# Kernel tuning notes

Hardware: AMD Instinct MI355X
Metric: run time of the kernel (lower is better)

The kernel has to match this reference:

```python
import jax, jax.numpy as jnp
import numpy as np
import math

GROUPS = 32  # min(256 // 4, 32)
EPS = 1e-5

def group_norm(x, w, b):
    B, C, H, W = x.shape
    xg = x.reshape(B, GROUPS, C // GROUPS, H, W)
    mean = jnp.mean(xg, axis=(2, 3, 4), keepdims=True)
    var = jnp.var(xg, axis=(2, 3, 4), keepdims=True)
    xn = ((xg - mean) * jax.lax.rsqrt(var + EPS)).reshape(B, C, H, W)
    return xn * w[None, :, None, None] + b[None, :, None, None]

def nin(x, W, b):
    # 1x1 projection: [B,C,H,W] x [C,D] -> [B,D,H,W]
    return jnp.einsum('bchw,cd->bdhw', x, W) + b[None, :, None, None]

def setup_inputs() -> dict:
    key = jax.random.key(0)
    ks = jax.random.split(key, 5)
    C = 256
    scale = 1.0 / math.sqrt(C)
    return {
        'x': jax.random.normal(ks[0], (4, C, 64, 64), dtype=jnp.float32),
        'gn_w': jnp.ones((C,), jnp.float32),
        'gn_b': jnp.zeros((C,), jnp.float32),
        'Wq': jax.random.normal(ks[1], (C, C), jnp.float32) * scale,
        'bq': jnp.zeros((C,), jnp.float32),
        'Wk': jax.random.normal(ks[2], (C, C), jnp.float32) * scale,
        'bk': jnp.zeros((C,), jnp.float32),
        'Wv': jax.random.normal(ks[3], (C, C), jnp.float32) * scale,
        'bv': jnp.zeros((C,), jnp.float32),
        'Wp': jax.random.normal(ks[4], (C, C), jnp.float32) * scale,
        'bp': jnp.zeros((C,), jnp.float32),
    }

def reference(x, gn_w, gn_b, Wq, bq, Wk, bk, Wv, bv, Wp, bp):
    B, C, H, W = x.shape
    h = group_norm(x, gn_w, gn_b)
    q = nin(h, Wq, bq).reshape(B, C, H * W)
    k = nin(h, Wk, bk).reshape(B, C, H * W)
    v = nin(h, Wv, bv).reshape(B, C, H * W)
    # attention logits: [B, HW, HW]
    w = jnp.einsum('bcn,bcm->bnm', q, k) * (C ** -0.5)
    w = jax.nn.softmax(w, axis=-1)
    h_out = jnp.einsum('bnm,bcm->bcn', w, v).reshape(B, C, H, W)
    h_out = nin(h_out, Wp, bp)
    out = x + h_out
    return out / math.sqrt(2.0)  # skip_rescale=True
```

## Files before the change

### kernel.cpp

```cpp
#include <hip/hip_runtime.h>
#include <math.h>


#define BB 4
#define CCH 256
#define NSP 4096
#define EPSV 1e-5f
#define ATTN_SCALE 0.0625f
#define RSQRT2 0.70710678118654752440f
#define KSPLIT 2
#define TILES_PER_PART 32

typedef __attribute__((ext_vector_type(8))) short bf16x8;
typedef __attribute__((ext_vector_type(4))) float f32x4;

typedef __attribute__((address_space(1))) void gvoid;
typedef __attribute__((address_space(3))) void lvoid;
__device__ __forceinline__ void dma16(const void* g, void* l) {
  __builtin_amdgcn_global_load_lds((gvoid*)g, (lvoid*)l, 16, 0, 0);
}

__device__ __forceinline__ short f2bf(float f) {
  union { float f; unsigned u; } a; a.f = f;
  unsigned r = a.u + 0x7fffu + ((a.u >> 16) & 1u);
  return (short)(r >> 16);
}
__device__ __forceinline__ float bf2f(short s) {
  union { unsigned u; float f; } a;
  a.u = ((unsigned)(unsigned short)s) << 16;
  return a.f;
}
__device__ __forceinline__ unsigned cvt_pk_bf16(float lo, float hi) {
  unsigned r;
  asm("v_cvt_pk_bf16_f32 %0, %1, %2" : "=v"(r) : "v"(lo), "v"(hi));
  return r;
}

__global__ __launch_bounds__(256) void gn_stats(
    const float* __restrict__ x, float* __restrict__ stats) {
  int b = blockIdx.x >> 5;
  int g = blockIdx.x & 31;
  size_t base = ((size_t)b * CCH + (size_t)g * 8) * NSP;
  const float4* xv = (const float4*)(x + base);
  int tid = threadIdx.x;
  float s = 0.f, ss = 0.f;
  for (int i = tid; i < 8192; i += 256) {
    float4 v = xv[i];
    s += (v.x + v.y) + (v.z + v.w);
    ss += (v.x * v.x + v.y * v.y) + (v.z * v.z + v.w * v.w);
  }
#pragma unroll
  for (int off = 32; off > 0; off >>= 1) {
    s += __shfl_down(s, off, 64);
    ss += __shfl_down(ss, off, 64);
  }
  __shared__ float rs[4], rss[4];
  int wv = tid >> 6;
  if ((tid & 63) == 0) { rs[wv] = s; rss[wv] = ss; }
  __syncthreads();
  if (tid == 0) {
    float S = rs[0] + rs[1] + rs[2] + rs[3];
    float SS = rss[0] + rss[1] + rss[2] + rss[3];
    float mean = S * (1.f / 32768.f);
    float var = SS * (1.f / 32768.f) - mean * mean;
    stats[(b * 32 + g) * 2 + 0] = mean;
    stats[(b * 32 + g) * 2 + 1] = rsqrtf(var + EPSV);
  }
}

__global__ __launch_bounds__(256) void prep_w(
    const float* __restrict__ Wq, const float* __restrict__ Wk,
    const float* __restrict__ Wv, const float* __restrict__ Wp,
    short* __restrict__ wts) {
  __shared__ float T[64][65];
  int c0 = blockIdx.x * 64, d0 = blockIdx.y * 64;
  int wz = blockIdx.z;
  const float* W = (wz == 0) ? Wq : (wz == 1) ? Wk : (wz == 2) ? Wv : Wp;
  short* wt = wts + (size_t)wz * CCH * CCH;
  int tid = threadIdx.x;
#pragma unroll
  for (int i = 0; i < 16; ++i) {
    int idx = tid + 256 * i;
    int row = idx >> 6, col = idx & 63;
    T[row][col] = W[(size_t)(c0 + row) * CCH + d0 + col];
  }
  __syncthreads();
#pragma unroll
  for (int i = 0; i < 16; ++i) {
    int idx = tid + 256 * i;
    int dr = idx >> 6, cc = idx & 63;
    wt[(size_t)(d0 + dr) * CCH + c0 + cc] = f2bf(T[cc][dr]);
  }
}

__global__ __launch_bounds__(256) void qkvg_kernel(
    const float* __restrict__ x, const float* __restrict__ stats,
    const float* __restrict__ gw, const float* __restrict__ gb,
    const short* __restrict__ wqt, const short* __restrict__ wkt,
    const short* __restrict__ wvt,
    const float* __restrict__ bq, const float* __restrict__ bk,
    const float* __restrict__ bv,
    short* __restrict__ qo, short* __restrict__ ko, short* __restrict__ vo) {
  __shared__ __align__(16) unsigned char smem[52224];
  float (*Ts)[68] = (float(*)[68])smem;
  float* aco = (float*)(smem + 17408);
  float* bco = aco + 256;
  short* Hs = (short*)(smem + 19456);
  short* Fo = (short*)smem;

  int bx = blockIdx.x;
  int b = bx & 3, n0 = (bx >> 2) * 64;
  int tid = threadIdx.x;
  {
    int g = tid >> 3;
    float mean = stats[(b * 32 + g) * 2 + 0];
    float rstd = stats[(b * 32 + g) * 2 + 1];
    float a = gw[tid] * rstd;
    aco[tid] = a;
    bco[tid] = gb[tid] - mean * a;
  }
  __syncthreads();
  const float* xb = x + (size_t)b * CCH * NSP;
  for (int p = 0; p < 4; ++p) {
    int c0 = p * 64;
#pragma unroll
    for (int i = 0; i < 4; ++i) {
      int crow = (tid >> 4) + i * 16;
      int c = c0 + crow;
      float4 v = *(const float4*)&xb[(size_t)c * NSP + n0 + (tid & 15) * 4];
      float a = aco[c], bb = bco[c];
      v.x = v.x * a + bb; v.y = v.y * a + bb;
      v.z = v.z * a + bb; v.w = v.w * a + bb;
      *(float4*)&Ts[crow][(tid & 15) * 4] = v;
    }
    __syncthreads();
    {
      int n = tid >> 2, seg = tid & 3;
#pragma unroll
      for (int u = 0; u < 2; ++u) {
        int cb = seg * 16 + u * 8;
        bf16x8 r;
#pragma unroll
        for (int j = 0; j < 8; ++j) r[j] = f2bf(Ts[cb + j][n]);
        int chunk = (c0 + cb) >> 3;
        *(bf16x8*)(Hs + n * 256 + ((chunk ^ (n & 7)) * 8)) = r;
      }
    }
    __syncthreads();
  }
  int w = tid >> 6, lane = tid & 63, quad = lane >> 4, l16 = lane & 15;
  bf16x8 a_h[8];
  {
    int row = w * 16 + l16;
#pragma unroll
    for (int kc = 0; kc < 8; ++kc)
      a_h[kc] = *(bf16x8*)(Hs + row * 256 + (((kc * 4 + quad) ^ (row & 7)) * 8));
  }
  __syncthreads();
  for (int op = 0; op < 3; ++op) {
    const short* wt = (op == 0) ? wqt : (op == 1) ? wkt : wvt;
    const float* bias = (op == 0) ? bq : (op == 1) ? bk : bv;
    f32x4 acc[16];
#pragma unroll
    for (int mb = 0; mb < 16; ++mb) acc[mb] = (f32x4){0.f, 0.f, 0.f, 0.f};
#pragma unroll 4
    for (int mb = 0; mb < 16; ++mb) {
      const short* wp = wt + (size_t)(mb * 16 + l16) * CCH + quad * 8;
#pragma unroll
      for (int kc = 0; kc < 8; ++kc) {
        bf16x8 af = *(const bf16x8*)(wp + kc * 32);
        acc[mb] = __builtin_amdgcn_mfma_f32_16x16x32_bf16(af, a_h[kc], acc[mb], 0, 0, 0);
      }
    }
    int n = n0 + w * 16 + l16;
    if (op == 2) {
      short* ob = vo + (size_t)b * CCH * NSP;
      int mm = n & 63, m0_ = n & ~63;
      int mb_ = mm >> 4, qq = (mm >> 2) & 3, rr2 = mm & 3;
      int lc = (mb_ & 1) * 4 + qq;
      int jj = (mb_ >> 1) * 4 + rr2;
      int basen = m0_ + jj;
#pragma unroll
      for (int mb = 0; mb < 16; ++mb)
#pragma unroll
        for (int r = 0; r < 4; ++r) {
          int d = mb * 16 + quad * 4 + r;
          ob[(size_t)d * NSP + basen + ((lc ^ (d & 7)) << 3)] =
              f2bf(acc[mb][r] + bias[d]);
        }
    } else {
      float sc = (op == 0) ? ATTN_SCALE : 1.f;
      int nl = w * 16 + l16;
#pragma unroll
      for (int mb = 0; mb < 16; ++mb)
#pragma unroll
        for (int r = 0; r < 4; ++r) {
          int d = mb * 16 + quad * 4 + r;
          Fo[nl * 264 + d] = f2bf((acc[mb][r] + bias[d]) * sc);
        }
      __syncthreads();
      short* ob = ((op == 0) ? qo : ko) + (size_t)b * NSP * CCH;
#pragma unroll
      for (int it = 0; it < 2; ++it) {
        int idx = tid + 256 * it;
        int row = idx >> 3, seg = idx & 7, r7 = row & 7;
        short* dst = ob + (size_t)(n0 + row) * CCH + seg * 32;
#pragma unroll
        for (int i = 0; i < 4; ++i) {
          int xch = seg * 4 + i;
          int cs = (xch & 24) | ((xch & 7) ^ r7);
          *(bf16x8*)(dst + i * 8) = *(bf16x8*)(Fo + row * 264 + cs * 8);
        }
      }
      __syncthreads();
    }
  }
}

__global__ __launch_bounds__(512, 1) void attn_kernel(
    const short* __restrict__ q, const short* __restrict__ k,
    const short* __restrict__ v, short* __restrict__ po,
    float* __restrict__ pm, float* __restrict__ pl) {
  __shared__ __align__(16) unsigned char smem[131072];
  short* Ks0 = (short*)smem;
  short* Ks1 = (short*)(smem + 32768);
  short* Vs0 = (short*)(smem + 65536);
  short* Vs1 = (short*)(smem + 98304);
  short* Fo  = (short*)smem;

  int bx = blockIdx.x;
  int b = bx & 3;
  int n0 = ((bx >> 2) & 31) << 7;
  int kh = bx >> 7;
  const short* qb = q + (size_t)b * NSP * CCH;
  const short* kb = k + (size_t)b * NSP * CCH;
  const char*  vbB = (const char*)(v + (size_t)b * CCH * NSP);
  int tid = threadIdx.x;
  int w = tid >> 6, lane = tid & 63, quad = lane >> 4, l16 = lane & 15;
  int mbase = kh * TILES_PER_PART * 64;

  bf16x8 a_q[8];
#pragma unroll
  for (int p = 0; p < 2; ++p) {
#pragma unroll
    for (int i = 0; i < 4; ++i) {
      int off = tid * 16 + i * 8192;
      dma16((const char*)(qb + (size_t)(n0 + p * 64) * CCH) + off,
            (char*)Ks0 + off);
    }
    __syncthreads();
    if ((w >> 2) == p) {
      int row = (w & 3) * 16 + l16;
#pragma unroll
      for (int kc = 0; kc < 8; ++kc)
        a_q[kc] = *(bf16x8*)(Ks0 + row * 256 + (((kc * 4 + quad) ^ (row & 7)) * 8));
    }
    __syncthreads();
  }

#pragma unroll
  for (int i = 0; i < 4; ++i) {
    int off = tid * 16 + i * 8192;
    dma16((const char*)(kb + (size_t)mbase * CCH) + off, (char*)Ks0 + off);
    int c = off >> 7, inrow = off & 127;
    dma16(vbB + (size_t)c * (NSP * 2) + (size_t)mbase * 2 + inrow,
          (char*)Vs0 + off);
  }
  __syncthreads();
#pragma unroll
  for (int i = 0; i < 4; ++i) {
    int off = tid * 16 + i * 8192;
    dma16((const char*)(kb + (size_t)(mbase + 64) * CCH) + off,
          (char*)Ks1 + off);
  }
  f32x4 s_prev[4];
#pragma unroll
  for (int mb = 0; mb < 4; ++mb) s_prev[mb] = (f32x4){0.f, 0.f, 0.f, 0.f};
  __builtin_amdgcn_s_setprio(1);
#pragma unroll
  for (int kc = 0; kc < 8; ++kc) {
#pragma unroll
    for (int mb = 0; mb < 4; ++mb) {
      int row = mb * 16 + l16;
      bf16x8 kf = *(bf16x8*)(Ks0 + row * 256 + (((kc * 4 + quad) ^ (row & 7)) * 8));
      s_prev[mb] = __builtin_amdgcn_mfma_f32_16x16x32_bf16(kf, a_q[kc], s_prev[mb], 0, 0, 0);
    }
  }
  __builtin_amdgcn_s_setprio(0);

  f32x4 accO[16];
#pragma unroll
  for (int cb = 0; cb < 16; ++cb) accO[cb] = (f32x4){0.f, 0.f, 0.f, 0.f};
  float m_run = -1e30f, l_run = 0.f;
  int pc0 = quad ^ (l16 & 7);
  int pc1 = (4 + quad) ^ (l16 & 7);

#pragma unroll 1
  for (int t = 0; t < TILES_PER_PART; ++t) {
    __syncthreads();
    short* Kd = (t & 1) ? Ks1 : Ks0;
    short* Kr = (t & 1) ? Ks0 : Ks1;
    short* Vd = (t & 1) ? Vs0 : Vs1;
    short* Vr = (t & 1) ? Vs1 : Vs0;
    if (t + 2 < TILES_PER_PART) {
      const char* kp = (const char*)(kb + (size_t)(mbase + (t + 2) * 64) * CCH);
#pragma unroll
      for (int i = 0; i < 4; ++i) {
        int off = tid * 16 + i * 8192;
        dma16(kp + off, (char*)Kd + off);
      }
    }
    if (t + 1 < TILES_PER_PART) {
      int m0 = mbase + (t + 1) * 64;
#pragma unroll
      for (int i = 0; i < 4; ++i) {
        int off = tid * 16 + i * 8192;
        int c = off >> 7, inrow = off & 127;
        dma16(vbB + (size_t)c * (NSP * 2) + (size_t)m0 * 2 + inrow,
              (char*)Vd + off);
      }
    }
    f32x4 sn[4];
#pragma unroll
    for (int mb = 0; mb < 4; ++mb) sn[mb] = (f32x4){0.f, 0.f, 0.f, 0.f};
    if (t + 1 < TILES_PER_PART) {
      __builtin_amdgcn_s_setprio(1);
#pragma unroll
      for (int kc = 0; kc < 8; ++kc) {
#pragma unroll
        for (int mb = 0; mb < 4; ++mb) {
          int row = mb * 16 + l16;
          bf16x8 kf = *(bf16x8*)(Kr + row * 256 + (((kc * 4 + quad) ^ (row & 7)) * 8));
          sn[mb] = __builtin_amdgcn_mfma_f32_16x16x32_bf16(kf, a_q[kc], sn[mb], 0, 0, 0);
        }
      }
      __builtin_amdgcn_s_setprio(0);
    }
    float mx = -1e30f;
#pragma unroll
    for (int mb = 0; mb < 4; ++mb)
#pragma unroll
      for (int r = 0; r < 4; ++r) mx = fmaxf(mx, s_prev[mb][r]);
    mx = fmaxf(mx, __shfl_xor(mx, 16));
    mx = fmaxf(mx, __shfl_xor(mx, 32));
    if (!__all(mx - m_run <= 8.f)) {
      float mnew = fmaxf(m_run, mx);
      float alpha = __expf(m_run - mnew);
#pragma unroll
      for (int cb = 0; cb < 16; ++cb) accO[cb] *= alpha;
      l_run *= alpha;
      m_run = mnew;
    }
    float ls = 0.f;
#pragma unroll
    for (int mb = 0; mb < 4; ++mb)
#pragma unroll
      for (int r = 0; r < 4; ++r) {
        float p = __expf(s_prev[mb][r] - m_run);
        ls += p;
        s_prev[mb][r] = p;
      }
    ls += __shfl_xor(ls, 16);
    ls += __shfl_xor(ls, 32);
    l_run += ls;
    union { unsigned u[4]; bf16x8 v; } pw0, pw1;
    pw0.u[0] = cvt_pk_bf16(s_prev[0][0], s_prev[0][1]);
    pw0.u[1] = cvt_pk_bf16(s_prev[0][2], s_prev[0][3]);
    pw0.u[2] = cvt_pk_bf16(s_prev[2][0], s_prev[2][1]);
    pw0.u[3] = cvt_pk_bf16(s_prev[2][2], s_prev[2][3]);
    pw1.u[0] = cvt_pk_bf16(s_prev[1][0], s_prev[1][1]);
    pw1.u[1] = cvt_pk_bf16(s_prev[1][2], s_prev[1][3]);
    pw1.u[2] = cvt_pk_bf16(s_prev[3][0], s_prev[3][1]);
    pw1.u[3] = cvt_pk_bf16(s_prev[3][2], s_prev[3][3]);
    __builtin_amdgcn_s_setprio(1);
#pragma unroll
    for (int cb = 0; cb < 16; ++cb) {
      bf16x8 vf = *(bf16x8*)(Vr + (cb * 16 + l16) * 64 + pc0 * 8);
      accO[cb] = __builtin_amdgcn_mfma_f32_16x16x32_bf16(vf, pw0.v, accO[cb], 0, 0, 0);
    }
#pragma unroll
    for (int cb = 0; cb < 16; ++cb) {
      bf16x8 vf = *(bf16x8*)(Vr + (cb * 16 + l16) * 64 + pc1 * 8);
      accO[cb] = __builtin_amdgcn_mfma_f32_16x16x32_bf16(vf, pw1.v, accO[cb], 0, 0, 0);
    }
    __builtin_amdgcn_s_setprio(0);
#pragma unroll
    for (int mb = 0; mb < 4; ++mb) s_prev[mb] = sn[mb];
  }
  size_t sbase = ((size_t)kh * BB + b) * NSP + n0;
  if (quad == 0) {
    pm[sbase + w * 16 + l16] = m_run;
    pl[sbase + w * 16 + l16] = l_run;
  }
  float linv = 1.f / l_run;
  short* ob = po + ((size_t)kh * BB + b) * NSP * CCH;
#pragma unroll
  for (int p = 0; p < 2; ++p) {
    __syncthreads();
    if ((w >> 2) == p) {
      int nloc = (w & 3) * 16 + l16;
#pragma unroll
      for (int cb = 0; cb < 16; ++cb)
#pragma unroll
        for (int r = 0; r < 4; ++r)
          Fo[nloc * 264 + cb * 16 + quad * 4 + r] = f2bf(accO[cb][r] * linv);
    }
    __syncthreads();
    int row = tid >> 3, seg = tid & 7;
    short* dst = ob + (size_t)(n0 + p * 64 + row) * CCH + seg * 32;
#pragma unroll
    for (int i = 0; i < 4; ++i)
      *(bf16x8*)(dst + i * 8) = *(bf16x8*)(Fo + row * 264 + seg * 32 + i * 8);
  }
}

__global__ __launch_bounds__(256) void proj_kernel(
    const short* __restrict__ po, const float* __restrict__ pm,
    const float* __restrict__ pl, const short* __restrict__ wpt,
    const float* __restrict__ bp, const float* __restrict__ x,
    float* __restrict__ out) {
  int n0 = blockIdx.x * 64;
  int dh = blockIdx.y * 128;
  int b = blockIdx.z;
  int tid = threadIdx.x;
  int w = tid >> 6, lane = tid & 63, quad = lane >> 4, l16 = lane & 15;
  int n = n0 + w * 16 + l16;

  float wgt[KSPLIT];
  {
    float m[KSPLIT];
    float M = -1e30f;
#pragma unroll
    for (int s = 0; s < KSPLIT; ++s) {
      m[s] = pm[((size_t)s * BB + b) * NSP + n];
      M = fmaxf(M, m[s]);
    }
    float wsum = 0.f;
#pragma unroll
    for (int s = 0; s < KSPLIT; ++s) {
      wgt[s] = __expf(m[s] - M) * pl[((size_t)s * BB + b) * NSP + n];
      wsum += wgt[s];
    }
    float linv = 1.f / wsum;
#pragma unroll
    for (int s = 0; s < KSPLIT; ++s) wgt[s] *= linv;
  }

  f32x4 acc[8];
#pragma unroll
  for (int mb = 0; mb < 8; ++mb) acc[mb] = (f32x4){0.f, 0.f, 0.f, 0.f};

  const short* pob = po + ((size_t)b * NSP + n) * CCH;
#pragma unroll 2
  for (int kc = 0; kc < 8; ++kc) {
    int coff = kc * 32 + quad * 8;
    float e[8];
#pragma unroll
    for (int i = 0; i < 8; ++i) e[i] = 0.f;
#pragma unroll
    for (int s = 0; s < KSPLIT; ++s) {
      bf16x8 f = *(const bf16x8*)(pob + (size_t)s * BB * NSP * CCH + coff);
#pragma unroll
      for (int i = 0; i < 8; ++i) e[i] += wgt[s] * bf2f(f[i]);
    }
    bf16x8 bm;
#pragma unroll
    for (int i = 0; i < 8; ++i) bm[i] = f2bf(e[i]);
#pragma unroll
    for (int mb = 0; mb < 8; ++mb) {
      bf16x8 af = *(const bf16x8*)(wpt + (size_t)(dh + mb * 16 + l16) * CCH + coff);
      acc[mb] = __builtin_amdgcn_mfma_f32_16x16x32_bf16(af, bm, acc[mb], 0, 0, 0);
    }
  }
#pragma unroll
  for (int mb = 0; mb < 8; ++mb) {
#pragma unroll
    for (int r = 0; r < 4; ++r) {
      int d = dh + mb * 16 + quad * 4 + r;
      size_t off = ((size_t)b * CCH + d) * NSP + n;
      out[off] = (acc[mb][r] + bp[d] + x[off]) * RSQRT2;
    }
  }
}

extern "C" void kernel_launch(void* const* d_in, const int* in_sizes, int n_in,
                              void* d_out, int out_size, void* d_ws, size_t ws_size,
                              hipStream_t stream) {
  const float* x  = (const float*)d_in[0];
  const float* gw = (const float*)d_in[1];
  const float* gb = (const float*)d_in[2];
  const float* Wq = (const float*)d_in[3];
  const float* bq = (const float*)d_in[4];
  const float* Wk = (const float*)d_in[5];
  const float* bk = (const float*)d_in[6];
  const float* Wv = (const float*)d_in[7];
  const float* bv = (const float*)d_in[8];
  const float* Wp = (const float*)d_in[9];
  const float* bp = (const float*)d_in[10];
  float* out = (float*)d_out;

  const size_t SZ = (size_t)BB * CCH * NSP;
  short* qb  = (short*)d_ws;
  short* kb  = qb + SZ;
  short* vb  = kb + SZ;
  short* poT = vb + SZ;
  float* pm  = (float*)(poT + (size_t)KSPLIT * SZ);
  float* pl  = pm + (size_t)KSPLIT * BB * NSP;
  float* stats = pl + (size_t)KSPLIT * BB * NSP;
  short* wts = (short*)(stats + BB * 64);
  short* wqt = wts;
  short* wkt = wts + (size_t)CCH * CCH;
  short* wvt = wts + (size_t)2 * CCH * CCH;
  short* wpt = wts + (size_t)3 * CCH * CCH;

  gn_stats<<<dim3(BB * 32), dim3(256), 0, stream>>>(x, stats);
  prep_w<<<dim3(4, 4, 4), dim3(256), 0, stream>>>(Wq, Wk, Wv, Wp, wts);
  qkvg_kernel<<<dim3(256), dim3(256), 0, stream>>>(
      x, stats, gw, gb, wqt, wkt, wvt, bq, bk, bv, qb, kb, vb);
  attn_kernel<<<dim3(BB * 32 * KSPLIT), dim3(512), 0, stream>>>(
      qb, kb, vb, poT, pm, pl);
  proj_kernel<<<dim3(64, 2, BB), dim3(256), 0, stream>>>(
      poT, pm, pl, wpt, bp, x, out);
}
```

Baseline: 282.9 us.

## Double qkvg threads, interleave attention split blocks, and hoist row-max computation

The QKV projection kernel now runs 512 threads per block, with each half of the waves computing half of the output channels. This halves per-thread accumulators and spreads the load and transpose work across more waves. The attention grid mapping is reordered so the two KV-split halves of the same batch and query tile are adjacent block IDs, which may improve cache sharing. The softmax row max for the next tile is now computed right after its QK MFMAs instead of at the top of the next iteration, shortening the critical path between dependent steps. Register pressure and occupancy of the projection kernel change and are hard to predict.

```diff
diff --git a/kernel.cpp b/kernel.cpp
--- a/kernel.cpp
+++ b/kernel.cpp
@@ -93,7 +93,7 @@
   }
 }
 
-__global__ __launch_bounds__(256) void qkvg_kernel(
+__global__ __launch_bounds__(512) void qkvg_kernel(
     const float* __restrict__ x, const float* __restrict__ stats,
     const float* __restrict__ gw, const float* __restrict__ gb,
     const short* __restrict__ wqt, const short* __restrict__ wkt,
@@ -111,7 +111,7 @@
   int bx = blockIdx.x;
   int b = bx & 3, n0 = (bx >> 2) * 64;
   int tid = threadIdx.x;
-  {
+  if (tid < 256) {
     int g = tid >> 3;
     float mean = stats[(b * 32 + g) * 2 + 0];
     float rstd = stats[(b * 32 + g) * 2 + 1];
@@ -124,8 +124,8 @@
   for (int p = 0; p < 4; ++p) {
     int c0 = p * 64;
 #pragma unroll
-    for (int i = 0; i < 4; ++i) {
-      int crow = (tid >> 4) + i * 16;
+    for (int i = 0; i < 2; ++i) {
+      int crow = (tid >> 4) + i * 32;
       int c = c0 + crow;
       float4 v = *(const float4*)&xb[(size_t)c * NSP + n0 + (tid & 15) * 4];
       float a = aco[c], bb = bco[c];
@@ -135,23 +135,21 @@
     }
     __syncthreads();
     {
-      int n = tid >> 2, seg = tid & 3;
-#pragma unroll
-      for (int u = 0; u < 2; ++u) {
-        int cb = seg * 16 + u * 8;
-        bf16x8 r;
-#pragma unroll
-        for (int j = 0; j < 8; ++j) r[j] = f2bf(Ts[cb + j][n]);
-        int chunk = (c0 + cb) >> 3;
-        *(bf16x8*)(Hs + n * 256 + ((chunk ^ (n & 7)) * 8)) = r;
-      }
+      int n = tid >> 3, seg = tid & 7;
+      int cb = seg * 8;
+      bf16x8 r;
+#pragma unroll
+      for (int j = 0; j < 8; ++j) r[j] = f2bf(Ts[cb + j][n]);
+      int chunk = (c0 + cb) >> 3;
+      *(bf16x8*)(Hs + n * 256 + ((chunk ^ (n & 7)) * 8)) = r;
     }
     __syncthreads();
   }
   int w = tid >> 6, lane = tid & 63, quad = lane >> 4, l16 = lane & 15;
+  int wr = w & 3, h = w >> 2;
   bf16x8 a_h[8];
   {
-    int row = w * 16 + l16;
+    int row = wr * 16 + l16;
 #pragma unroll
     for (int kc = 0; kc < 8; ++kc)
       a_h[kc] = *(bf16x8*)(Hs + row * 256 + (((kc * 4 + quad) ^ (row & 7)) * 8));
@@ -160,19 +158,19 @@
   for (int op = 0; op < 3; ++op) {
     const short* wt = (op == 0) ? wqt : (op == 1) ? wkt : wvt;
     const float* bias = (op == 0) ? bq : (op == 1) ? bk : bv;
-    f32x4 acc[16];
-#pragma unroll
-    for (int mb = 0; mb < 16; ++mb) acc[mb] = (f32x4){0.f, 0.f, 0.f, 0.f};
+    f32x4 acc[8];
+#pragma unroll
+    for (int mb = 0; mb < 8; ++mb) acc[mb] = (f32x4){0.f, 0.f, 0.f, 0.f};
 #pragma unroll 4
-    for (int mb = 0; mb < 16; ++mb) {
-      const short* wp = wt + (size_t)(mb * 16 + l16) * CCH + quad * 8;
+    for (int mb = 0; mb < 8; ++mb) {
+      const short* wp = wt + (size_t)((h * 8 + mb) * 16 + l16) * CCH + quad * 8;
 #pragma unroll
       for (int kc = 0; kc < 8; ++kc) {
         bf16x8 af = *(const bf16x8*)(wp + kc * 32);
         acc[mb] = __builtin_amdgcn_mfma_f32_16x16x32_bf16(af, a_h[kc], acc[mb], 0, 0, 0);
       }
     }
-    int n = n0 + w * 16 + l16;
+    int n = n0 + wr * 16 + l16;
     if (op == 2) {
       short* ob = vo + (size_t)b * CCH * NSP;
       int mm = n & 63, m0_ = n & ~63;
@@ -181,29 +179,27 @@
       int jj = (mb_ >> 1) * 4 + rr2;
       int basen = m0_ + jj;
 #pragma unroll
-      for (int mb = 0; mb < 16; ++mb)
+      for (int mb = 0; mb < 8; ++mb)
 #pragma unroll
         for (int r = 0; r < 4; ++r) {
-          int d = mb * 16 + quad * 4 + r;
+          int d = (h * 8 + mb) * 16 + quad * 4 + r;
           ob[(size_t)d * NSP + basen + ((lc ^ (d & 7)) << 3)] =
               f2bf(acc[mb][r] + bias[d]);
         }
     } else {
       float sc = (op == 0) ? ATTN_SCALE : 1.f;
-      int nl = w * 16 + l16;
-#pragma unroll
-      for (int mb = 0; mb < 16; ++mb)
+      int nl = wr * 16 + l16;
+#pragma unroll
+      for (int mb = 0; mb < 8; ++mb)
 #pragma unroll
         for (int r = 0; r < 4; ++r) {
-          int d = mb * 16 + quad * 4 + r;
+          int d = (h * 8 + mb) * 16 + quad * 4 + r;
           Fo[nl * 264 + d] = f2bf((acc[mb][r] + bias[d]) * sc);
         }
       __syncthreads();
       short* ob = ((op == 0) ? qo : ko) + (size_t)b * NSP * CCH;
-#pragma unroll
-      for (int it = 0; it < 2; ++it) {
-        int idx = tid + 256 * it;
-        int row = idx >> 3, seg = idx & 7, r7 = row & 7;
+      {
+        int row = tid >> 3, seg = tid & 7, r7 = row & 7;
         short* dst = ob + (size_t)(n0 + row) * CCH + seg * 32;
 #pragma unroll
         for (int i = 0; i < 4; ++i) {
@@ -229,9 +225,10 @@
   short* Fo  = (short*)smem;
 
   int bx = blockIdx.x;
-  int b = bx & 3;
-  int n0 = ((bx >> 2) & 31) << 7;
-  int kh = bx >> 7;
+  int grp = bx & 7;
+  int b = grp & 3;
+  int kh = grp >> 2;
+  int n0 = ((bx >> 3) & 31) << 7;
   const short* qb = q + (size_t)b * NSP * CCH;
   const short* kb = k + (size_t)b * NSP * CCH;
   const char*  vbB = (const char*)(v + (size_t)b * CCH * NSP);
@@ -287,6 +284,13 @@
     }
   }
   __builtin_amdgcn_s_setprio(0);
+  float mx_c = -1e30f;
+#pragma unroll
+  for (int mb = 0; mb < 4; ++mb)
+#pragma unroll
+    for (int r = 0; r < 4; ++r) mx_c = fmaxf(mx_c, s_prev[mb][r]);
+  mx_c = fmaxf(mx_c, __shfl_xor(mx_c, 16));
+  mx_c = fmaxf(mx_c, __shfl_xor(mx_c, 32));
 
   f32x4 accO[16];
 #pragma unroll
@@ -336,15 +340,8 @@
       }
       __builtin_amdgcn_s_setprio(0);
     }
-    float mx = -1e30f;
-#pragma unroll
-    for (int mb = 0; mb < 4; ++mb)
-#pragma unroll
-      for (int r = 0; r < 4; ++r) mx = fmaxf(mx, s_prev[mb][r]);
-    mx = fmaxf(mx, __shfl_xor(mx, 16));
-    mx = fmaxf(mx, __shfl_xor(mx, 32));
-    if (!__all(mx - m_run <= 8.f)) {
-      float mnew = fmaxf(m_run, mx);
+    if (!__all(mx_c - m_run <= 8.f)) {
+      float mnew = fmaxf(m_run, mx_c);
       float alpha = __expf(m_run - mnew);
 #pragma unroll
       for (int cb = 0; cb < 16; ++cb) accO[cb] *= alpha;
@@ -384,6 +381,16 @@
       accO[cb] = __builtin_amdgcn_mfma_f32_16x16x32_bf16(vf, pw1.v, accO[cb], 0, 0, 0);
     }
     __builtin_amdgcn_s_setprio(0);
+    if (t + 1 < TILES_PER_PART) {
+      float mxn = -1e30f;
+#pragma unroll
+      for (int mb = 0; mb < 4; ++mb)
+#pragma unroll
+        for (int r = 0; r < 4; ++r) mxn = fmaxf(mxn, sn[mb][r]);
+      mxn = fmaxf(mxn, __shfl_xor(mxn, 16));
+      mxn = fmaxf(mxn, __shfl_xor(mxn, 32));
+      mx_c = mxn;
+    }
 #pragma unroll
     for (int mb = 0; mb < 4; ++mb) s_prev[mb] = sn[mb];
   }
@@ -515,7 +522,7 @@
 
   gn_stats<<<dim3(BB * 32), dim3(256), 0, stream>>>(x, stats);
   prep_w<<<dim3(4, 4, 4), dim3(256), 0, stream>>>(Wq, Wk, Wv, Wp, wts);
-  qkvg_kernel<<<dim3(256), dim3(256), 0, stream>>>(
+  qkvg_kernel<<<dim3(256), dim3(512), 0, stream>>>(
       x, stats, gw, gb, wqt, wkt, wvt, bq, bk, bv, qb, kb, vb);
   attn_kernel<<<dim3(BB * 32 * KSPLIT), dim3(512), 0, stream>>>(
       qb, kb, vb, poT, pm, pl);
```

New measurement: 275.4 us. 2.6% less time.
